# Optimization experiments

Measured on AMD Instinct MI355X. Metric: run time of the kernel, lower is better.

## Reference

```python
import jax, jax.numpy as jnp
import numpy as np

NUM_HEADS = 16

def setup_inputs() -> dict:
    key = jax.random.key(0)
    ks = jax.random.split(key, 5)
    d_model = 1024
    x = jax.random.normal(ks[0], (2, 2048, d_model), dtype=jnp.float32)
    # xavier-uniform-like scale for square [d_model, d_model] weights
    lim = float(np.sqrt(6.0 / (d_model + d_model)))
    def w(k):
        return jax.random.uniform(k, (d_model, d_model), dtype=jnp.float32, minval=-lim, maxval=lim)
    return {"x": x, "Wq": w(ks[1]), "Wk": w(ks[2]), "Wv": w(ks[3]), "Wo": w(ks[4])}

def reference(x, Wq, Wk, Wv, Wo):
    B, S, D = x.shape
    H = NUM_HEADS
    dk = D // H
    # project: torch does x @ W.T
    def split_heads(t):
        return t.reshape(B, S, H, dk).transpose(0, 2, 1, 3)  # [B,H,S,dk]
    q = split_heads(x @ Wq.T)
    k = split_heads(x @ Wk.T)
    v = split_heads(x @ Wv.T)
    scores = jnp.einsum('bhqd,bhkd->bhqk', q, k) / jnp.sqrt(jnp.float32(dk))
    causal = jnp.tril(jnp.ones((S, S), dtype=bool))  # True where attended
    scores = jnp.where(causal[None, None], scores, -jnp.inf)
    probs = jax.nn.softmax(scores, axis=-1)
    out = jnp.einsum('bhqk,bhkd->bhqd', probs, v)  # [B,H,S,dk]
    out = out.transpose(0, 2, 1, 3).reshape(B, S, D)
    return out @ Wo.T
```

## Files before the change

### kernel.cpp

```cpp
#include <hip/hip_runtime.h>
#include <stdint.h>

#define BATCH  2
#define SEQ    2048
#define DMODEL 1024
#define NHEADS 16
#define DKH    64
#define MTOT   (BATCH*SEQ)
#define VSTR   (SEQ + 32)

typedef unsigned short u16;
typedef __bf16 bf16x8 __attribute__((ext_vector_type(8)));
typedef float  f32x4  __attribute__((ext_vector_type(4)));

extern "C" __device__ float __ocml_native_exp2_f32(float);

__device__ __forceinline__ u16 f2bf(float f) {
  union { float f; uint32_t u; } v; v.f = f;
  uint32_t u = v.u;
  return (u16)((u + 0x7FFFu + ((u >> 16) & 1u)) >> 16);
}
__device__ __forceinline__ float bf2f(u16 h) {
  union { uint32_t u; float f; } v; v.u = (uint32_t)h << 16; return v.f;
}

__device__ __forceinline__ void gld_lds16(const void* g, void* l) {
  __builtin_amdgcn_global_load_lds(
      (__attribute__((address_space(1))) void*)g,
      (__attribute__((address_space(3))) void*)l, 16, 0, 0);
}

__device__ __forceinline__ uint32_t cvtpk(float lo, float hi) {
  uint32_t r;
  asm("v_cvt_pk_bf16_f32 %0, %1, %2" : "=v"(r) : "v"(lo), "v"(hi));
  return r;
}
__device__ __forceinline__ void pl16swap(uint32_t& a, uint32_t& b) {
  asm volatile("v_permlane16_swap_b32 %0, %1" : "+v"(a), "+v"(b));
}

__global__ void cvt_f32_bf16(const float* __restrict__ src, u16* __restrict__ dst) {
  size_t i = ((size_t)blockIdx.x * 256 + threadIdx.x) * 4;
  float4 f = *(const float4*)(src + i);
  ushort4 o;
  o.x = f2bf(f.x); o.y = f2bf(f.y); o.z = f2bf(f.z); o.w = f2bf(f.w);
  *(ushort4*)(dst + i) = o;
}
__global__ void cvt_w(const float* __restrict__ a, const float* __restrict__ b,
                      const float* __restrict__ c, const float* __restrict__ d,
                      u16* __restrict__ dst) {
  const float* srcs[4] = {a, b, c, d};
  const float* s = srcs[blockIdx.y];
  size_t i = ((size_t)blockIdx.x * 256 + threadIdx.x) * 4;
  float4 f = *(const float4*)(s + i);
  ushort4 o;
  o.x = f2bf(f.x); o.y = f2bf(f.y); o.z = f2bf(f.z); o.w = f2bf(f.w);
  *(ushort4*)(dst + (size_t)blockIdx.y * (DMODEL*DMODEL) + i) = o;
}

__global__ __launch_bounds__(256, 3) void gemm_qkv(
    const u16* __restrict__ xb, const u16* __restrict__ wq,
    const u16* __restrict__ wk, const u16* __restrict__ wv,
    u16* __restrict__ q, u16* __restrict__ k, u16* __restrict__ v, float qscale) {
  __shared__ __align__(16) u16 lA[128 * 64];
  __shared__ __align__(16) u16 lB[3][64 * 64];

  const int tid  = threadIdx.x;
  const int lane = tid & 63;
  const int lrow = lane & 15;
  const int quad = lane >> 4;
  const int wave = tid >> 6;
  const int wm   = (wave & 1) * 64;
  const int wn   = (wave >> 1) * 32;
  const int sx   = lrow & 7;
  const int m0 = blockIdx.x * 128, n0 = blockIdx.y * 64;
  const u16* Ws[3] = {wq, wk, wv};

  f32x4 acc[3][4][2] = {};

  for (int k0 = 0; k0 < DMODEL; k0 += 64) {
    #pragma unroll
    for (int r = 0; r < 4; ++r) {
      int off  = r * 4096 + tid * 16;
      int row  = off >> 7;
      int c16  = (off >> 4) & 7;
      int colb = (c16 ^ (row & 7)) << 4;
      gld_lds16((const char*)xb + ((size_t)(m0 + row) * DMODEL + k0) * 2 + colb,
                (char*)lA + off);
    }
    #pragma unroll
    for (int z = 0; z < 3; ++z)
      #pragma unroll
      for (int r = 0; r < 2; ++r) {
        int off  = r * 4096 + tid * 16;
        int row  = off >> 7;
        int c16  = (off >> 4) & 7;
        int colb = (c16 ^ (row & 7)) << 4;
        gld_lds16((const char*)Ws[z] + ((size_t)(n0 + row) * DMODEL + k0) * 2 + colb,
                  (char*)&lB[z][0] + off);
      }
    __syncthreads();
    #pragma unroll
    for (int ks = 0; ks < 2; ++ks) {
      const int ro = ((((ks << 2) | quad) ^ sx) << 3);
      bf16x8 a[4], b[3][2];
      #pragma unroll
      for (int i = 0; i < 4; ++i)
        a[i] = *(const bf16x8*)(lA + (wm + i*16 + lrow) * 64 + ro);
      #pragma unroll
      for (int z = 0; z < 3; ++z)
        #pragma unroll
        for (int j = 0; j < 2; ++j)
          b[z][j] = *(const bf16x8*)(&lB[z][0] + (wn + j*16 + lrow) * 64 + ro);
      #pragma unroll
      for (int z = 0; z < 3; ++z)
        #pragma unroll
        for (int i = 0; i < 4; ++i)
          #pragma unroll
          for (int j = 0; j < 2; ++j)
            acc[z][i][j] = __builtin_amdgcn_mfma_f32_16x16x32_bf16(a[i], b[z][j], acc[z][i][j], 0, 0, 0);
    }
    __syncthreads();
  }

  const int rb = quad * 4, cb = lrow;
  const int h  = blockIdx.y;
  u16* outs[3] = {q, k, v};
  #pragma unroll
  for (int z = 0; z < 3; ++z) {
    u16* out = outs[z];
    if (z == 2) {
      #pragma unroll
      for (int i = 0; i < 4; ++i)
        #pragma unroll
        for (int j = 0; j < 2; ++j) {
          int row0 = m0 + wm + i*16 + rb;
          int d_   = wn + j*16 + cb;
          int b_ = row0 >> 11, s0 = row0 & 2047;
          ushort4 pk;
          pk.x = f2bf(acc[z][i][j][0]); pk.y = f2bf(acc[z][i][j][1]);
          pk.z = f2bf(acc[z][i][j][2]); pk.w = f2bf(acc[z][i][j][3]);
          *(ushort4*)&out[((size_t)(b_*NHEADS + h) * DKH + d_) * VSTR + s0] = pk;
        }
    } else {
      const float scale = (z == 0) ? qscale : 1.0f;
      #pragma unroll
      for (int i = 0; i < 4; ++i)
        #pragma unroll
        for (int j = 0; j < 2; ++j)
          #pragma unroll
          for (int r = 0; r < 4; ++r) {
            int row = m0 + wm + i*16 + rb + r;
            int d_  = wn + j*16 + cb;
            int b_ = row >> 11, s_ = row & 2047;
            out[(((size_t)(b_*NHEADS + h) * SEQ + s_) << 6) + d_] =
                f2bf(acc[z][i][j][r] * scale);
          }
    }
  }
}

__device__ __forceinline__ void gemm_core64(const u16* A, const u16* W,
                                            int m0, int n0, f32x4 acc[4][2],
                                            u16* lA, u16* lB) {
  const int tid  = threadIdx.x;
  const int lane = tid & 63;
  const int lrow = lane & 15;
  const int quad = lane >> 4;
  const int wave = tid >> 6;
  const int wm   = (wave & 1) * 64;
  const int wn   = (wave >> 1) * 32;
  const int sx   = lrow & 7;

  for (int k0 = 0; k0 < DMODEL; k0 += 64) {
    #pragma unroll
    for (int r = 0; r < 4; ++r) {
      int off  = r * 4096 + tid * 16;
      int row  = off >> 7;
      int c16  = (off >> 4) & 7;
      int colb = (c16 ^ (row & 7)) << 4;
      gld_lds16((const char*)A + ((size_t)(m0 + row) * DMODEL + k0) * 2 + colb,
                (char*)lA + off);
    }
    #pragma unroll
    for (int r = 0; r < 2; ++r) {
      int off  = r * 4096 + tid * 16;
      int row  = off >> 7;
      int c16  = (off >> 4) & 7;
      int colb = (c16 ^ (row & 7)) << 4;
      gld_lds16((const char*)W + ((size_t)(n0 + row) * DMODEL + k0) * 2 + colb,
                (char*)lB + off);
    }
    __syncthreads();
    #pragma unroll
    for (int ks = 0; ks < 2; ++ks) {
      bf16x8 a[4], b[2];
      const int ro = ((((ks << 2) | quad) ^ sx) << 3);
      #pragma unroll
      for (int i = 0; i < 4; ++i)
        a[i] = *(const bf16x8*)(lA + (wm + i*16 + lrow) * 64 + ro);
      #pragma unroll
      for (int j = 0; j < 2; ++j)
        b[j] = *(const bf16x8*)(lB + (wn + j*16 + lrow) * 64 + ro);
      #pragma unroll
      for (int i = 0; i < 4; ++i)
        #pragma unroll
        for (int j = 0; j < 2; ++j)
          acc[i][j] = __builtin_amdgcn_mfma_f32_16x16x32_bf16(a[i], b[j], acc[i][j], 0, 0, 0);
    }
    __syncthreads();
  }
}

__global__ __launch_bounds__(256, 3) void gemm_out(
    const u16* __restrict__ ab, const u16* __restrict__ wo, float* __restrict__ out) {
  __shared__ __align__(16) u16 lA[128 * 64];
  __shared__ __align__(16) u16 lB[64 * 64];
  const int m0 = blockIdx.x * 128, n0 = blockIdx.y * 64;
  f32x4 acc[4][2] = {};
  gemm_core64(ab, wo, m0, n0, acc, lA, lB);

  const int lane = threadIdx.x & 63;
  const int wave = threadIdx.x >> 6;
  const int wm = (wave & 1) * 64, wn = (wave >> 1) * 32;
  const int rb = (lane >> 4) * 4, cb = lane & 15;
  #pragma unroll
  for (int i = 0; i < 4; ++i)
    #pragma unroll
    for (int j = 0; j < 2; ++j)
      #pragma unroll
      for (int r = 0; r < 4; ++r)
        out[(size_t)(m0 + wm + i*16 + rb + r) * DMODEL + (n0 + wn + j*16 + cb)]
            = acc[i][j][r];
}

__device__ const uint8_t JT[80] = {
  124,125,126,127, 120,121,122, 116,117,118, 112,113,114, 108,109,110,
  104,105,106, 100,101,102, 96,97,98, 92,93,94, 88,89, 84,85, 80,81,
  76,77, 72,73, 68,69, 64,65, 60,61, 56, 52, 48, 44, 40, 36, 32, 28,
  123,90,57,24, 119,86,53,20, 115,82,49,16, 111,78,45,12,
  107,74,41,8, 103,70,37,4, 99,66,33,0
};

__device__ __forceinline__ void stage_kv(const u16* Kg, const u16* Vg, int t,
                                         u16* lK, u16* lV, int tid) {
  #pragma unroll
  for (int r = 0; r < 2; ++r) {
    int off  = r * 4096 + tid * 16;
    int row  = off >> 7;
    int colb = (((off >> 4) & 7) ^ (row & 7)) << 4;
    gld_lds16((const char*)Kg + ((size_t)(t*64 + row) * DKH) * 2 + colb,
              (char*)lK + off);
    gld_lds16((const char*)Vg + ((size_t)row * VSTR + t*64) * 2 + colb,
              (char*)lV + off);
  }
}

__global__ __launch_bounds__(256, 4) void attn(
    const u16* __restrict__ Q, const u16* __restrict__ K,
    const u16* __restrict__ V, u16* __restrict__ O,
    u16* __restrict__ po, float* __restrict__ pl) {
  __shared__ __align__(16) u16 lK[2][64 * 64];
  __shared__ __align__(16) u16 lV[2][64 * 64];

  const int tid  = threadIdx.x;
  const int wid  = tid >> 6;
  const int lane = tid & 63;
  const int lrow = lane & 15;
  const int quad = lane >> 4;
  const int sx   = lrow & 7;
  const int pq   = ((quad & 1) << 1) | (quad >> 1);

  const int g  = blockIdx.x >> 5;
  const int bh = blockIdx.x & 31;
  const int e  = JT[g];
  const int p  = e >> 2, c = e & 3;
  const int lo = c * 8;
  const int hi = (p + 1 < lo + 8) ? p + 1 : lo + 8;

  const u16* Qg = Q + (size_t)bh * SEQ * DKH;
  const u16* Kg = K + (size_t)bh * SEQ * DKH;
  const u16* Vg = V + (size_t)bh * DKH * VSTR;

  bf16x8 aq[2];
  #pragma unroll
  for (int ks = 0; ks < 2; ++ks)
    aq[ks] = *(const bf16x8*)(Qg + (size_t)(64*p + 16*wid + lrow) * DKH + ks*32 + quad*8);

  f32x4 o_acc[4] = {};
  float l_acc = 0.f;

  stage_kv(Kg, Vg, lo, &lK[0][0], &lV[0][0], tid);
  __syncthreads();
  int cur = 0;

  for (int t = lo; t < hi; ++t) {
    if (t + 1 < hi)
      stage_kv(Kg, Vg, t + 1, &lK[cur ^ 1][0], &lV[cur ^ 1][0], tid);

    bf16x8 kf[2][4], vf[2][4];
    #pragma unroll
    for (int ks = 0; ks < 2; ++ks) {
      const int kro = ((((ks << 2) | quad) ^ sx) << 3);
      const int vro = ((((ks << 2) | pq)   ^ sx) << 3);
      #pragma unroll
      for (int j = 0; j < 4; ++j) {
        kf[ks][j] = *(const bf16x8*)(&lK[cur][0] + (j*16 + lrow) * 64 + kro);
        vf[ks][j] = *(const bf16x8*)(&lV[cur][0] + (j*16 + lrow) * 64 + vro);
      }
    }

    f32x4 s_acc[4] = {};
    #pragma unroll
    for (int ks = 0; ks < 2; ++ks)
      #pragma unroll
      for (int j = 0; j < 4; ++j)
        s_acc[j] = __builtin_amdgcn_mfma_f32_16x16x32_bf16(kf[ks][j], aq[ks], s_acc[j], 0, 0, 0);

    if (t == p) {
      const int qloc = 16*wid + lrow;
      #pragma unroll
      for (int j = 0; j < 4; ++j) {
        int kl = j*16 + quad*4;
        #pragma unroll
        for (int r = 0; r < 4; ++r)
          if (kl + r > qloc) s_acc[j][r] = -1e30f;
      }
    }

    uint32_t w[4][2];
    float ls = 0.f;
    #pragma unroll
    for (int j = 0; j < 4; ++j) {
      float p0 = __ocml_native_exp2_f32(s_acc[j][0]);
      float p1 = __ocml_native_exp2_f32(s_acc[j][1]);
      float p2 = __ocml_native_exp2_f32(s_acc[j][2]);
      float p3 = __ocml_native_exp2_f32(s_acc[j][3]);
      ls += (p0 + p1) + (p2 + p3);
      w[j][0] = cvtpk(p0, p1);
      w[j][1] = cvtpk(p2, p3);
    }
    l_acc += ls;

    pl16swap(w[0][0], w[1][0]);
    pl16swap(w[0][1], w[1][1]);
    pl16swap(w[2][0], w[3][0]);
    pl16swap(w[2][1], w[3][1]);
    union { uint32_t u[4]; bf16x8 v; } g0, g1;
    g0.u[0] = w[0][0]; g0.u[1] = w[0][1]; g0.u[2] = w[1][0]; g0.u[3] = w[1][1];
    g1.u[0] = w[2][0]; g1.u[1] = w[2][1]; g1.u[2] = w[3][0]; g1.u[3] = w[3][1];

    #pragma unroll
    for (int j = 0; j < 4; ++j)
      o_acc[j] = __builtin_amdgcn_mfma_f32_16x16x32_bf16(g0.v, vf[0][j], o_acc[j], 0, 0, 0);
    #pragma unroll
    for (int j = 0; j < 4; ++j)
      o_acc[j] = __builtin_amdgcn_mfma_f32_16x16x32_bf16(g1.v, vf[1][j], o_acc[j], 0, 0, 0);

    __syncthreads();
    cur ^= 1;
  }

  float lr[4];
  {
    float s = l_acc;
    s += __shfl_xor(s, 16, 64);
    s += __shfl_xor(s, 32, 64);
    #pragma unroll
    for (int r = 0; r < 4; ++r)
      lr[r] = __shfl(s, quad*4 + r, 16);
  }

  if (p <= 7) {
    const int h = bh & 15, b_ = bh >> 4;
    #pragma unroll
    for (int j = 0; j < 4; ++j)
      #pragma unroll
      for (int r = 0; r < 4; ++r) {
        int sg = 64*p + 16*wid + quad*4 + r;
        O[(size_t)(b_ * SEQ + sg) * DMODEL + h * DKH + j*16 + lrow]
            = f2bf(o_acc[j][r] / lr[r]);
      }
  } else {
    const int base = (p < 16) ? (p - 8) * 2
                   : (p < 24) ? 16 + (p - 16) * 3
                   :            40 + (p - 24) * 4;
    const int slot = (base + c) * 32 + bh;
    #pragma unroll
    for (int j = 0; j < 4; ++j) {
      ushort4 pk;
      pk.x = f2bf(o_acc[j][0]); pk.y = f2bf(o_acc[j][1]);
      pk.z = f2bf(o_acc[j][2]); pk.w = f2bf(o_acc[j][3]);
      *(ushort4*)&po[(size_t)slot * 4096 + (j*16 + lrow) * 64 + 16*wid + quad*4] = pk;
    }
    if (lrow == 0)
      #pragma unroll
      for (int r = 0; r < 4; ++r)
        pl[slot * 64 + 16*wid + quad*4 + r] = lr[r];
  }
}

__global__ __launch_bounds__(256) void combine(
    const u16* __restrict__ po, const float* __restrict__ pl, u16* __restrict__ ab) {
  __shared__ u16 Ls[64][68];
  const int b  = blockIdx.x;
  const int p  = 8 + (b >> 5);
  const int bh = b & 31;
  const int t  = threadIdx.x;
  const int col = t >> 2;
  const int r0  = (t & 3) * 16;
  const int base = (p < 16) ? (p - 8) * 2
                 : (p < 24) ? 16 + (p - 16) * 3
                 :            40 + (p - 24) * 4;
  const int nc   = (p < 16) ? 2 : (p < 24) ? 3 : 4;

  float acc[16], lsum[16];
  const size_t s0 = (size_t)(base * 32 + bh);
  const u16*   q0 = po + s0 * 4096 + col * 64 + r0;
  const float* l0 = pl + s0 * 64 + r0;
  #pragma unroll
  for (int q4 = 0; q4 < 4; ++q4) {
    ushort4 a  = *(const ushort4*)(q0 + q4 * 4);
    ushort4 c2 = *(const ushort4*)(q0 + (size_t)32 * 4096 + q4 * 4);
    acc[q4*4+0] = bf2f(a.x) + bf2f(c2.x);
    acc[q4*4+1] = bf2f(a.y) + bf2f(c2.y);
    acc[q4*4+2] = bf2f(a.z) + bf2f(c2.z);
    acc[q4*4+3] = bf2f(a.w) + bf2f(c2.w);
    float4 f = *(const float4*)(l0 + q4 * 4);
    float4 g = *(const float4*)(l0 + 32 * 64 + q4 * 4);
    lsum[q4*4+0] = f.x + g.x; lsum[q4*4+1] = f.y + g.y;
    lsum[q4*4+2] = f.z + g.z; lsum[q4*4+3] = f.w + g.w;
  }
  if (nc >= 3) {
    #pragma unroll
    for (int q4 = 0; q4 < 4; ++q4) {
      ushort4 a = *(const ushort4*)(q0 + (size_t)64 * 4096 + q4 * 4);
      acc[q4*4+0] += bf2f(a.x); acc[q4*4+1] += bf2f(a.y);
      acc[q4*4+2] += bf2f(a.z); acc[q4*4+3] += bf2f(a.w);
      float4 f = *(const float4*)(l0 + 64 * 64 + q4 * 4);
      lsum[q4*4+0] += f.x; lsum[q4*4+1] += f.y;
      lsum[q4*4+2] += f.z; lsum[q4*4+3] += f.w;
    }
  }
  if (nc == 4) {
    #pragma unroll
    for (int q4 = 0; q4 < 4; ++q4) {
      ushort4 a = *(const ushort4*)(q0 + (size_t)96 * 4096 + q4 * 4);
      acc[q4*4+0] += bf2f(a.x); acc[q4*4+1] += bf2f(a.y);
      acc[q4*4+2] += bf2f(a.z); acc[q4*4+3] += bf2f(a.w);
      float4 f = *(const float4*)(l0 + 96 * 64 + q4 * 4);
      lsum[q4*4+0] += f.x; lsum[q4*4+1] += f.y;
      lsum[q4*4+2] += f.z; lsum[q4*4+3] += f.w;
    }
  }
  #pragma unroll
  for (int q = 0; q < 16; ++q)
    Ls[r0 + q][col] = f2bf(acc[q] / lsum[q]);
  __syncthreads();

  const int row = t >> 2;
  const int c0  = (t & 3) * 16;
  const int b_ = bh >> 4, h = bh & 15;
  u16* dst = ab + (size_t)(b_ * SEQ + 64 * p + row) * DMODEL + h * DKH + c0;
  #pragma unroll
  for (int q = 0; q < 16; q += 4)
    *(ushort4*)(dst + q) = *(const ushort4*)&Ls[row][c0 + q];
}

extern "C" void kernel_launch(void* const* d_in, const int* in_sizes, int n_in,
                              void* d_out, int out_size, void* d_ws, size_t ws_size,
                              hipStream_t stream) {
  const float* x  = (const float*)d_in[0];
  const float* Wq = (const float*)d_in[1];
  const float* Wk = (const float*)d_in[2];
  const float* Wv = (const float*)d_in[3];
  const float* Wo = (const float*)d_in[4];
  float* out = (float*)d_out;

  u16* xb  = (u16*)d_ws;
  u16* wqb = xb  + (size_t)MTOT * DMODEL;
  u16* wkb = wqb + (size_t)DMODEL * DMODEL;
  u16* wvb = wkb + (size_t)DMODEL * DMODEL;
  u16* wob = wvb + (size_t)DMODEL * DMODEL;
  u16* qb  = wob + (size_t)DMODEL * DMODEL;
  u16* kb  = qb  + (size_t)MTOT * DMODEL;
  u16* vb  = kb  + (size_t)MTOT * DMODEL;
  u16* ab  = vb  + (size_t)BATCH * NHEADS * DKH * VSTR;
  u16* po  = ab  + (size_t)MTOT * DMODEL;
  float* pl = (float*)(po + (size_t)2304 * 4096);

  cvt_f32_bf16<<<MTOT * DMODEL / 1024, 256, 0, stream>>>(x, xb);
  cvt_w<<<dim3(DMODEL * DMODEL / 1024, 4), 256, 0, stream>>>(Wq, Wk, Wv, Wo, wqb);

  const float qscale = 0.125f * 1.44269504088896340736f;
  gemm_qkv<<<dim3(32, 16), 256, 0, stream>>>(
      xb, wqb, wkb, wvb, qb, kb, vb, qscale);

  attn<<<2560, 256, 0, stream>>>(qb, kb, vb, ab, po, pl);
  combine<<<768, 256, 0, stream>>>(po, pl, ab);

  gemm_out<<<dim3(32, 16), 256, 0, stream>>>(ab, wob, out);
}
```

Measured before the change: 167.2 us.

## Process 128 query rows per attention block to halve K/V staging

Each attention block now covers 128 query rows instead of 64, with every wave handling two 16-row query tiles against the same staged K/V tile. This halves the number of blocks and the K/V loads from global memory into LDS per query row. The split-KV work table, causal masking and partial-output slot mapping are rewritten for the larger tile. In exchange, register use per thread roughly doubles for accumulators, occupancy hints drop from 4 to 2 blocks per SIMD, and fewer blocks means coarser load balancing.

```diff
diff --git a/kernel.cpp b/kernel.cpp
--- a/kernel.cpp
+++ b/kernel.cpp
@@ -234,12 +234,10 @@
             = acc[i][j][r];
 }
 
-__device__ const uint8_t JT[80] = {
-  124,125,126,127, 120,121,122, 116,117,118, 112,113,114, 108,109,110,
-  104,105,106, 100,101,102, 96,97,98, 92,93,94, 88,89, 84,85, 80,81,
-  76,77, 72,73, 68,69, 64,65, 60,61, 56, 52, 48, 44, 40, 36, 32, 28,
-  123,90,57,24, 119,86,53,20, 115,82,49,16, 111,78,45,12,
-  107,74,41,8, 103,70,37,4, 99,66,33,0
+__device__ const uint8_t JT[40] = {
+  60,61,62,63, 56,57,58, 52,53,54, 48,49,50, 44,45,46, 40,41, 36,37,
+  32,33, 28,29, 24, 20, 16, 12,
+  59,42,25,8, 55,38,21,4, 51,34,17,0
 };
 
 __device__ __forceinline__ void stage_kv(const u16* Kg, const u16* Vg, int t,
@@ -256,7 +254,7 @@
   }
 }
 
-__global__ __launch_bounds__(256, 4) void attn(
+__global__ __launch_bounds__(256, 2) void attn(
     const u16* __restrict__ Q, const u16* __restrict__ K,
     const u16* __restrict__ V, u16* __restrict__ O,
     u16* __restrict__ po, float* __restrict__ pl) {
@@ -274,21 +272,26 @@
   const int g  = blockIdx.x >> 5;
   const int bh = blockIdx.x & 31;
   const int e  = JT[g];
-  const int p  = e >> 2, c = e & 3;
+  const int u  = e >> 2, c = e & 3;
   const int lo = c * 8;
-  const int hi = (p + 1 < lo + 8) ? p + 1 : lo + 8;
+  const int T  = 2*u + 2;
+  const int hi = (lo + 8 < T) ? lo + 8 : T;
+  const int td = 2*u + (wid >> 1);
+  const int qg0 = 128*u + 32*wid;
 
   const u16* Qg = Q + (size_t)bh * SEQ * DKH;
   const u16* Kg = K + (size_t)bh * SEQ * DKH;
   const u16* Vg = V + (size_t)bh * DKH * VSTR;
 
-  bf16x8 aq[2];
-  #pragma unroll
-  for (int ks = 0; ks < 2; ++ks)
-    aq[ks] = *(const bf16x8*)(Qg + (size_t)(64*p + 16*wid + lrow) * DKH + ks*32 + quad*8);
-
-  f32x4 o_acc[4] = {};
-  float l_acc = 0.f;
+  bf16x8 aq[2][2];
+  #pragma unroll
+  for (int i = 0; i < 2; ++i)
+    #pragma unroll
+    for (int ks = 0; ks < 2; ++ks)
+      aq[i][ks] = *(const bf16x8*)(Qg + (size_t)(qg0 + 16*i + lrow) * DKH + ks*32 + quad*8);
+
+  f32x4 o_acc[2][4] = {};
+  float l_acc[2] = {};
 
   stage_kv(Kg, Vg, lo, &lK[0][0], &lV[0][0], tid);
   __syncthreads();
@@ -310,93 +313,104 @@
       }
     }
 
-    f32x4 s_acc[4] = {};
-    #pragma unroll
-    for (int ks = 0; ks < 2; ++ks)
+    #pragma unroll
+    for (int i = 0; i < 2; ++i) {
+      f32x4 s_acc[4] = {};
+      #pragma unroll
+      for (int ks = 0; ks < 2; ++ks)
+        #pragma unroll
+        for (int j = 0; j < 4; ++j)
+          s_acc[j] = __builtin_amdgcn_mfma_f32_16x16x32_bf16(kf[ks][j], aq[i][ks], s_acc[j], 0, 0, 0);
+
+      if (t >= td) {
+        const int qrel = qg0 + 16*i + lrow - 64*t;
+        #pragma unroll
+        for (int j = 0; j < 4; ++j) {
+          int kl = j*16 + quad*4;
+          #pragma unroll
+          for (int r = 0; r < 4; ++r)
+            if (kl + r > qrel) s_acc[j][r] = -1e30f;
+        }
+      }
+
+      uint32_t w[4][2];
+      float ls = 0.f;
+      #pragma unroll
+      for (int j = 0; j < 4; ++j) {
+        float p0 = __ocml_native_exp2_f32(s_acc[j][0]);
+        float p1 = __ocml_native_exp2_f32(s_acc[j][1]);
+        float p2 = __ocml_native_exp2_f32(s_acc[j][2]);
+        float p3 = __ocml_native_exp2_f32(s_acc[j][3]);
+        ls += (p0 + p1) + (p2 + p3);
+        w[j][0] = cvtpk(p0, p1);
+        w[j][1] = cvtpk(p2, p3);
+      }
+      l_acc[i] += ls;
+
+      pl16swap(w[0][0], w[1][0]);
+      pl16swap(w[0][1], w[1][1]);
+      pl16swap(w[2][0], w[3][0]);
+      pl16swap(w[2][1], w[3][1]);
+      union { uint32_t u[4]; bf16x8 v; } g0, g1;
+      g0.u[0] = w[0][0]; g0.u[1] = w[0][1]; g0.u[2] = w[1][0]; g0.u[3] = w[1][1];
+      g1.u[0] = w[2][0]; g1.u[1] = w[2][1]; g1.u[2] = w[3][0]; g1.u[3] = w[3][1];
+
       #pragma unroll
       for (int j = 0; j < 4; ++j)
-        s_acc[j] = __builtin_amdgcn_mfma_f32_16x16x32_bf16(kf[ks][j], aq[ks], s_acc[j], 0, 0, 0);
-
-    if (t == p) {
-      const int qloc = 16*wid + lrow;
-      #pragma unroll
-      for (int j = 0; j < 4; ++j) {
-        int kl = j*16 + quad*4;
-        #pragma unroll
-        for (int r = 0; r < 4; ++r)
-          if (kl + r > qloc) s_acc[j][r] = -1e30f;
-      }
-    }
-
-    uint32_t w[4][2];
-    float ls = 0.f;
-    #pragma unroll
-    for (int j = 0; j < 4; ++j) {
-      float p0 = __ocml_native_exp2_f32(s_acc[j][0]);
-      float p1 = __ocml_native_exp2_f32(s_acc[j][1]);
-      float p2 = __ocml_native_exp2_f32(s_acc[j][2]);
-      float p3 = __ocml_native_exp2_f32(s_acc[j][3]);
-      ls += (p0 + p1) + (p2 + p3);
-      w[j][0] = cvtpk(p0, p1);
-      w[j][1] = cvtpk(p2, p3);
-    }
-    l_acc += ls;
-
-    pl16swap(w[0][0], w[1][0]);
-    pl16swap(w[0][1], w[1][1]);
-    pl16swap(w[2][0], w[3][0]);
-    pl16swap(w[2][1], w[3][1]);
-    union { uint32_t u[4]; bf16x8 v; } g0, g1;
-    g0.u[0] = w[0][0]; g0.u[1] = w[0][1]; g0.u[2] = w[1][0]; g0.u[3] = w[1][1];
-    g1.u[0] = w[2][0]; g1.u[1] = w[2][1]; g1.u[2] = w[3][0]; g1.u[3] = w[3][1];
-
-    #pragma unroll
-    for (int j = 0; j < 4; ++j)
-      o_acc[j] = __builtin_amdgcn_mfma_f32_16x16x32_bf16(g0.v, vf[0][j], o_acc[j], 0, 0, 0);
-    #pragma unroll
-    for (int j = 0; j < 4; ++j)
-      o_acc[j] = __builtin_amdgcn_mfma_f32_16x16x32_bf16(g1.v, vf[1][j], o_acc[j], 0, 0, 0);
+        o_acc[i][j] = __builtin_amdgcn_mfma_f32_16x16x32_bf16(g0.v, vf[0][j], o_acc[i][j], 0, 0, 0);
+      #pragma unroll
+      for (int j = 0; j < 4; ++j)
+        o_acc[i][j] = __builtin_amdgcn_mfma_f32_16x16x32_bf16(g1.v, vf[1][j], o_acc[i][j], 0, 0, 0);
+    }
 
     __syncthreads();
     cur ^= 1;
   }
 
-  float lr[4];
-  {
-    float s = l_acc;
+  float lr[2][4];
+  #pragma unroll
+  for (int i = 0; i < 2; ++i) {
+    float s = l_acc[i];
     s += __shfl_xor(s, 16, 64);
     s += __shfl_xor(s, 32, 64);
     #pragma unroll
     for (int r = 0; r < 4; ++r)
-      lr[r] = __shfl(s, quad*4 + r, 16);
-  }
-
-  if (p <= 7) {
+      lr[i][r] = __shfl(s, quad*4 + r, 16);
+  }
+
+  if (T <= 8) {
     const int h = bh & 15, b_ = bh >> 4;
     #pragma unroll
-    for (int j = 0; j < 4; ++j)
-      #pragma unroll
-      for (int r = 0; r < 4; ++r) {
-        int sg = 64*p + 16*wid + quad*4 + r;
-        O[(size_t)(b_ * SEQ + sg) * DMODEL + h * DKH + j*16 + lrow]
-            = f2bf(o_acc[j][r] / lr[r]);
+    for (int i = 0; i < 2; ++i)
+      #pragma unroll
+      for (int j = 0; j < 4; ++j)
+        #pragma unroll
+        for (int r = 0; r < 4; ++r) {
+          int sg = qg0 + 16*i + quad*4 + r;
+          O[(size_t)(b_ * SEQ + sg) * DMODEL + h * DKH + j*16 + lrow]
+              = f2bf(o_acc[i][j][r] / lr[i][r]);
+        }
+  } else {
+    const int pold = td;
+    const int base = (pold < 16) ? (pold - 8) * 2
+                   : (pold < 24) ? 16 + (pold - 16) * 3
+                   :               40 + (pold - 24) * 4;
+    const int slot = (base + c) * 32 + bh;
+    const int r64  = 32 * (wid & 1);
+    #pragma unroll
+    for (int i = 0; i < 2; ++i) {
+      #pragma unroll
+      for (int j = 0; j < 4; ++j) {
+        ushort4 pk;
+        pk.x = f2bf(o_acc[i][j][0]); pk.y = f2bf(o_acc[i][j][1]);
+        pk.z = f2bf(o_acc[i][j][2]); pk.w = f2bf(o_acc[i][j][3]);
+        *(ushort4*)&po[(size_t)slot * 4096 + (j*16 + lrow) * 64 + r64 + 16*i + quad*4] = pk;
       }
-  } else {
-    const int base = (p < 16) ? (p - 8) * 2
-                   : (p < 24) ? 16 + (p - 16) * 3
-                   :            40 + (p - 24) * 4;
-    const int slot = (base + c) * 32 + bh;
-    #pragma unroll
-    for (int j = 0; j < 4; ++j) {
-      ushort4 pk;
-      pk.x = f2bf(o_acc[j][0]); pk.y = f2bf(o_acc[j][1]);
-      pk.z = f2bf(o_acc[j][2]); pk.w = f2bf(o_acc[j][3]);
-      *(ushort4*)&po[(size_t)slot * 4096 + (j*16 + lrow) * 64 + 16*wid + quad*4] = pk;
-    }
-    if (lrow == 0)
-      #pragma unroll
-      for (int r = 0; r < 4; ++r)
-        pl[slot * 64 + 16*wid + quad*4 + r] = lr[r];
+      if (lrow == 0)
+        #pragma unroll
+        for (int r = 0; r < 4; ++r)
+          pl[slot * 64 + r64 + 16*i + quad*4 + r] = lr[i][r];
+    }
   }
 }
 
@@ -496,7 +510,7 @@
   gemm_qkv<<<dim3(32, 16), 256, 0, stream>>>(
       xb, wqb, wkb, wvb, qb, kb, vb, qscale);
 
-  attn<<<2560, 256, 0, stream>>>(qb, kb, vb, ab, po, pl);
+  attn<<<1280, 256, 0, stream>>>(qb, kb, vb, ab, po, pl);
   combine<<<768, 256, 0, stream>>>(po, pl, ab);
 
   gemm_out<<<dim3(32, 16), 256, 0, stream>>>(ab, wob, out);
```

Measured after the change: 164.3 us. Within noise of the previous version (-1.7%).
